# Kernel optimization log

Measured on AMD Instinct MI355X. Metric: run time of the kernel, lower is better.

The kernel has to match this reference:

```python
import jax, jax.numpy as jnp
import numpy as np

TOP_K = 4
N_GROUP = 4
TOPK_GROUP = 2
ROUTED_SCALING = 1.0


def setup_inputs() -> dict:
    key = jax.random.key(0)
    k1, k2, k3, k4, k5 = jax.random.split(key, 5)
    B, S, H, I, E = 1, 2048, 1024, 512, 16
    hidden_states = jax.random.normal(k1, (B, S, H), dtype=jnp.float32)
    # router weight (kaiming-uniform-like scale)
    gate_weight = jax.random.normal(k2, (E, H), dtype=jnp.float32) * (1.0 / np.sqrt(H))
    e_bias = jnp.zeros((E,), dtype=jnp.float32)  # e_score_correction_bias buffer
    gate_proj = jax.random.normal(k3, (E, I, H), dtype=jnp.float32) * 0.02
    up_proj = jax.random.normal(k4, (E, I, H), dtype=jnp.float32) * 0.02
    down_proj = jax.random.normal(k5, (E, H, I), dtype=jnp.float32) * 0.02
    return {
        "hidden_states": hidden_states,
        "gate_weight": gate_weight,
        "e_bias": e_bias,
        "gate_proj": gate_proj,
        "up_proj": up_proj,
        "down_proj": down_proj,
    }


def _route(x_flat, gate_weight, e_bias):
    # x_flat: [T, H]
    T = x_flat.shape[0]
    E = gate_weight.shape[0]
    logits = jnp.einsum("th,eh->te", x_flat, gate_weight)
    scores = jax.nn.sigmoid(logits)                      # [T, E]
    scores_for_choice = scores + e_bias[None, :]
    # group scores = sum of top-2 expert scores within each group
    grp = scores_for_choice.reshape(T, N_GROUP, E // N_GROUP)
    top2, _ = jax.lax.top_k(grp, 2)
    group_scores = top2.sum(axis=-1)                     # [T, G]
    _, group_idx = jax.lax.top_k(group_scores, TOPK_GROUP)
    group_mask = jax.nn.one_hot(group_idx, N_GROUP, dtype=scores.dtype).sum(axis=1)  # [T, G]
    score_mask = jnp.repeat(group_mask, E // N_GROUP, axis=1)                        # [T, E]
    tmp_scores = jnp.where(score_mask > 0, scores_for_choice, 0.0)
    _, topk_idx = jax.lax.top_k(tmp_scores, TOP_K)       # [T, K]
    topk_weight = jnp.take_along_axis(scores, topk_idx, axis=1)
    denom = topk_weight.sum(axis=-1, keepdims=True) + 1e-20
    topk_weight = topk_weight / denom * ROUTED_SCALING
    return topk_idx, topk_weight


def reference(hidden_states, gate_weight, e_bias, gate_proj, up_proj, down_proj):
    B, S, H = hidden_states.shape
    E = gate_proj.shape[0]
    x = hidden_states.reshape(-1, H).astype(jnp.float32)  # [T, H]
    topk_idx, topk_weight = _route(x, gate_weight, e_bias)
    # combine weights per (token, expert): sum over the k slots selecting e
    combine = (jax.nn.one_hot(topk_idx, E, dtype=x.dtype) * topk_weight[..., None]).sum(axis=1)  # [T, E]
    # dense expert MLP (mathematically equal to gather-compute-scatter since
    # non-selected experts receive zero combine weight)
    g = jnp.einsum("th,eih->tei", x, gate_proj)
    u = jnp.einsum("th,eih->tei", x, up_proj)
    act = jax.nn.silu(g) * u                              # [T, E, I]
    expert_out = jnp.einsum("tei,ehi->teh", act, down_proj)
    y = jnp.einsum("teh,te->th", expert_out, combine)
    return y.reshape(B, S, H)
```

## Files before the change

### kernel.cpp

```cpp
#include <hip/hip_runtime.h>
#include <hip/hip_bf16.h>

typedef __attribute__((ext_vector_type(8))) short bf16x8;
typedef __attribute__((ext_vector_type(4))) float f32x4;

#define T_TOK 2048
#define HD 1024
#define ID 512
#define NE 16
#define TOPK 4
#define BK 64
#define WELEM (HD*ID*NE)

__device__ __forceinline__ unsigned pk2(float a, float b) {
    return __builtin_amdgcn_perm(__float_as_uint(b), __float_as_uint(a),
                                 0x07060302u);
}
__device__ __forceinline__ bf16x8 cvt8(const float* __restrict__ p) {
    float4 a = *(const float4*)p;
    float4 b = *(const float4*)(p + 4);
    union { bf16x8 v; unsigned u[4]; } r;
    r.u[0] = pk2(a.x, a.y); r.u[1] = pk2(a.z, a.w);
    r.u[2] = pk2(b.x, b.y); r.u[3] = pk2(b.z, b.w);
    return r.v;
}
__device__ __forceinline__ short f2bf(float f) {
    unsigned u = __float_as_uint(f);
    return (short)((u + 0x7fffu + ((u >> 16) & 1u)) >> 16);
}

#define MFMA_BF16 __builtin_amdgcn_mfma_f32_16x16x32_bf16

__global__ __launch_bounds__(256) void conv_k(const float* __restrict__ src,
                                              short* __restrict__ dst) {
    size_t i = ((size_t)blockIdx.x * 256 + threadIdx.x) * 8;
    union { bf16x8 v; uint4 q; } r;
    r.v = cvt8(src + i);
    *(uint4*)(dst + i) = r.q;
}

__global__ __launch_bounds__(256) void router_k(
        const float* __restrict__ x, const float* __restrict__ gw,
        const float* __restrict__ eb,
        int* __restrict__ tk_idx, float* __restrict__ tk_w,
        short* __restrict__ xb) {
    int wid  = (blockIdx.x * 256 + threadIdx.x) >> 6;
    int lane = threadIdx.x & 63;

    const float* xr = x + (size_t)wid * HD + lane * 16;
    float xv[16];
#pragma unroll
    for (int c = 0; c < 4; c++) {
        float4 v = *(const float4*)(xr + c * 4);
        xv[4 * c] = v.x; xv[4 * c + 1] = v.y; xv[4 * c + 2] = v.z; xv[4 * c + 3] = v.w;
    }
    {
        union { uint4 q; unsigned u[4]; } w0, w1;
        w0.u[0] = pk2(xv[0], xv[1]);  w0.u[1] = pk2(xv[2], xv[3]);
        w0.u[2] = pk2(xv[4], xv[5]);  w0.u[3] = pk2(xv[6], xv[7]);
        w1.u[0] = pk2(xv[8], xv[9]);  w1.u[1] = pk2(xv[10], xv[11]);
        w1.u[2] = pk2(xv[12], xv[13]); w1.u[3] = pk2(xv[14], xv[15]);
        short* d = xb + ((size_t)wid << 10) + lane * 16;
        *(uint4*)d = w0.q;
        *(uint4*)(d + 8) = w1.q;
    }

    float logits[NE];
#pragma unroll
    for (int e = 0; e < NE; e++) {
        const float* gr = gw + e * HD + lane * 16;
        float p = 0.f;
#pragma unroll
        for (int c = 0; c < 4; c++) {
            float4 v = *(const float4*)(gr + c * 4);
            p += xv[4 * c] * v.x + xv[4 * c + 1] * v.y +
                 xv[4 * c + 2] * v.z + xv[4 * c + 3] * v.w;
        }
#pragma unroll
        for (int s = 32; s > 0; s >>= 1) p += __shfl_xor(p, s, 64);
        logits[e] = p;
    }

    float scores[NE], sc[NE];
#pragma unroll
    for (int e = 0; e < NE; e++) {
        scores[e] = 1.f / (1.f + __expf(-logits[e]));
        sc[e] = scores[e] + eb[e];
    }

    float gs[4];
#pragma unroll
    for (int g = 0; g < 4; g++) {
        float a = sc[4 * g], b = sc[4 * g + 1], c = sc[4 * g + 2], d = sc[4 * g + 3];
        float h1 = fmaxf(a, b), l1 = fminf(a, b);
        float h2 = fmaxf(c, d), l2 = fminf(c, d);
        gs[g] = fmaxf(h1, h2) + fmaxf(fminf(h1, h2), fmaxf(l1, l2));
    }
    int g0 = 0; float b0 = gs[0];
#pragma unroll
    for (int g = 1; g < 4; g++) if (gs[g] > b0) { b0 = gs[g]; g0 = g; }
    int g1 = -1; float b1 = -1e30f;
#pragma unroll
    for (int g = 0; g < 4; g++) if (g != g0 && gs[g] > b1) { b1 = gs[g]; g1 = g; }

    int taken = 0;
    int bid[TOPK]; float bsc[TOPK]; float wsum = 0.f;
#pragma unroll
    for (int k = 0; k < TOPK; k++) {
        float bv = -1e30f; int bi = 0; float bs = 0.f;
#pragma unroll
        for (int e = 0; e < NE; e++) {
            int grp = e >> 2;
            bool ok = ((grp == g0) || (grp == g1)) && !((taken >> e) & 1);
            if (ok && sc[e] > bv) { bv = sc[e]; bi = e; bs = scores[e]; }
        }
        taken |= (1 << bi);
        bid[k] = bi; bsc[k] = bs; wsum += bs;
    }
    if (lane == 0) {
        float inv = 1.0f / (wsum + 1e-20f);
#pragma unroll
        for (int k = 0; k < TOPK; k++) {
            tk_idx[wid * TOPK + k] = bid[k];
            tk_w[wid * TOPK + k]   = bsc[k] * inv;
        }
    }
}

__global__ __launch_bounds__(256) void assign_k(
        const int* __restrict__ tk_idx,
        int* __restrict__ counts, int* __restrict__ tok_list,
        int* __restrict__ pair_slot) {
    int p = blockIdx.x * 256 + threadIdx.x;
    int e = tk_idx[p];
    int slot = atomicAdd(&counts[e], 1);
    tok_list[e * T_TOK + slot] = p >> 2;
    pair_slot[p] = slot;
}

__global__ void offs_k(const int* __restrict__ counts, int* __restrict__ offs) {
    if (threadIdx.x == 0) {
        int a = 0;
#pragma unroll
        for (int e = 0; e < NE; e++) { offs[e] = a; a += counts[e]; }
    }
}

__global__ __launch_bounds__(256) void gemm1_k(
        const short* __restrict__ xb,
        const short* __restrict__ gpb,
        const short* __restrict__ upb,
        const int* __restrict__ counts,
        const int* __restrict__ offs,
        const int* __restrict__ tok_list,
        short* __restrict__ act) {
    __shared__ short xs[128 * BK];
    __shared__ short gs[64 * BK];
    __shared__ short us[64 * BK];
    __shared__ int   tok_s[128];

    int e = blockIdx.z;
    int cnt = counts[e];
    int base = blockIdx.y * 128;
    if (base >= cnt) return;
    int arow0 = offs[e] + base;

    int tid = threadIdx.x;
    if (tid < 128) {
        int s = base + tid;
        tok_s[tid] = (s < cnt) ? tok_list[e * T_TOK + s] : tok_list[e * T_TOK];
    }

    int wv = tid >> 6, lane = tid & 63;
    int qd = lane >> 4, l16 = lane & 15;
    int wm = (wv >> 1) * 64, wn = (wv & 1) * 32;
    int nb0 = blockIdx.x * 64;
    const short* gp = gpb + (size_t)e * ID * HD + (size_t)nb0 * HD;
    const short* up = upb + (size_t)e * ID * HD + (size_t)nb0 * HD;

    f32x4 accg[4][2] = {};
    f32x4 accu[4][2] = {};
    __syncthreads();

    for (int kp = 0; kp < HD; kp += BK) {
#pragma unroll
        for (int i = 0; i < 4; i++) {
            int idx = i * 256 + tid;
            int r = idx >> 3, c = idx & 7;
            *(uint4*)&xs[(r << 6) + (((c ^ r) & 7) << 3)] =
                *(const uint4*)(xb + ((size_t)tok_s[r] << 10) + kp + (c << 3));
        }
#pragma unroll
        for (int i = 0; i < 2; i++) {
            int idx = i * 256 + tid;
            int r = idx >> 3, c = idx & 7;
            size_t go = (size_t)r * HD + kp + (c << 3);
            int lo = (r << 6) + (((c ^ r) & 7) << 3);
            *(uint4*)&gs[lo] = *(const uint4*)(gp + go);
            *(uint4*)&us[lo] = *(const uint4*)(up + go);
        }
        __syncthreads();
#pragma unroll
        for (int ks = 0; ks < 2; ks++) {
            int cb = ks * 4 + qd;
            bf16x8 af[4], bg[2], bu[2];
#pragma unroll
            for (int i = 0; i < 4; i++) {
                int r = wm + i * 16 + l16;
                af[i] = *(const bf16x8*)&xs[(r << 6) + (((cb ^ r) & 7) << 3)];
            }
#pragma unroll
            for (int j = 0; j < 2; j++) {
                int r = wn + j * 16 + l16;
                int lo = (r << 6) + (((cb ^ r) & 7) << 3);
                bg[j] = *(const bf16x8*)&gs[lo];
                bu[j] = *(const bf16x8*)&us[lo];
            }
#pragma unroll
            for (int i = 0; i < 4; i++)
#pragma unroll
                for (int j = 0; j < 2; j++) {
                    accg[i][j] = MFMA_BF16(af[i], bg[j], accg[i][j], 0, 0, 0);
                    accu[i][j] = MFMA_BF16(af[i], bu[j], accu[i][j], 0, 0, 0);
                }
        }
        __syncthreads();
    }

#pragma unroll
    for (int i = 0; i < 4; i++)
#pragma unroll
        for (int j = 0; j < 2; j++)
#pragma unroll
            for (int r = 0; r < 4; r++) {
                int m = wm + i * 16 + qd * 4 + r;
                if (base + m < cnt) {
                    float g = accg[i][j][r], u = accu[i][j][r];
                    float a = g / (1.f + __expf(-g)) * u;
                    act[(size_t)(arow0 + m) * ID + nb0 + wn + j * 16 + l16] = f2bf(a);
                }
            }
}

__global__ __launch_bounds__(256) void gemm2_k(
        const short* __restrict__ act,
        const short* __restrict__ dpb,
        const int* __restrict__ counts,
        const int* __restrict__ offs,
        float* __restrict__ yexp) {
    __shared__ short as_[128 * BK];
    __shared__ short ds_[128 * BK];

    int e = blockIdx.z;
    int cnt = counts[e];
    int base = blockIdx.y * 128;
    if (base >= cnt) return;
    int arow0 = offs[e] + base;

    int tid = threadIdx.x;
    int wv = tid >> 6, lane = tid & 63;
    int qd = lane >> 4, l16 = lane & 15;
    int wm = (wv >> 1) * 64, wn = (wv & 1) * 64;
    int hb0 = blockIdx.x * 128;
    const short* dp = dpb + (size_t)e * HD * ID + (size_t)hb0 * ID;

    f32x4 acc[4][4] = {};
    __syncthreads();

    for (int kp = 0; kp < ID; kp += BK) {
#pragma unroll
        for (int i = 0; i < 4; i++) {
            int idx = i * 256 + tid;
            int r = idx >> 3, c = idx & 7;
            int lo = (r << 6) + (((c ^ r) & 7) << 3);
            *(uint4*)&as_[lo] =
                *(const uint4*)(act + (size_t)(arow0 + r) * ID + kp + (c << 3));
            *(uint4*)&ds_[lo] =
                *(const uint4*)(dp + (size_t)r * ID + kp + (c << 3));
        }
        __syncthreads();
#pragma unroll
        for (int ks = 0; ks < 2; ks++) {
            int cb = ks * 4 + qd;
            bf16x8 af[4], bd[4];
#pragma unroll
            for (int i = 0; i < 4; i++) {
                int r = wm + i * 16 + l16;
                af[i] = *(const bf16x8*)&as_[(r << 6) + (((cb ^ r) & 7) << 3)];
                int r2 = wn + i * 16 + l16;
                bd[i] = *(const bf16x8*)&ds_[(r2 << 6) + (((cb ^ r2) & 7) << 3)];
            }
#pragma unroll
            for (int i = 0; i < 4; i++)
#pragma unroll
                for (int j = 0; j < 4; j++)
                    acc[i][j] = MFMA_BF16(af[i], bd[j], acc[i][j], 0, 0, 0);
        }
        __syncthreads();
    }

#pragma unroll
    for (int i = 0; i < 4; i++)
#pragma unroll
        for (int j = 0; j < 4; j++)
#pragma unroll
            for (int r = 0; r < 4; r++) {
                int m = wm + i * 16 + qd * 4 + r;
                if (base + m < cnt)
                    yexp[(size_t)(arow0 + m) * HD + hb0 + wn + j * 16 + l16] =
                        acc[i][j][r];
            }
}

__global__ __launch_bounds__(256) void combine_k(
        const float* __restrict__ yexp,
        const int* __restrict__ offs,
        const int* __restrict__ tk_idx, const float* __restrict__ tk_w,
        const int* __restrict__ pair_slot,
        float* __restrict__ out) {
    int t = blockIdx.x, i = threadIdx.x;
    float4 acc = {0.f, 0.f, 0.f, 0.f};
#pragma unroll
    for (int k = 0; k < TOPK; k++) {
        int p = t * TOPK + k;
        int e = tk_idx[p];
        int row = offs[e] + pair_slot[p];
        float w = tk_w[p];
        float4 v = *(const float4*)(yexp + (size_t)row * HD + (i << 2));
        acc.x += w * v.x; acc.y += w * v.y;
        acc.z += w * v.z; acc.w += w * v.w;
    }
    *(float4*)(out + (size_t)t * HD + (i << 2)) = acc;
}

extern "C" void kernel_launch(void* const* d_in, const int* in_sizes, int n_in,
                              void* d_out, int out_size, void* d_ws, size_t ws_size,
                              hipStream_t stream) {
    const float* x  = (const float*)d_in[0];
    const float* gw = (const float*)d_in[1];
    const float* eb = (const float*)d_in[2];
    const float* gp = (const float*)d_in[3];
    const float* up = (const float*)d_in[4];
    const float* dp = (const float*)d_in[5];

    short* gpb = (short*)d_ws;
    short* upb = gpb + WELEM;
    short* dpb = upb + WELEM;
    short* xb  = dpb + WELEM;
    short* act = xb + (size_t)T_TOK * HD;
    int* counts    = (int*)(act + (size_t)(T_TOK * TOPK + 128) * ID);
    int* offs      = counts + NE;
    int* tok_list  = offs + NE;
    int* pair_slot = tok_list + NE * T_TOK;
    int* tk_idx    = pair_slot + T_TOK * TOPK;
    float* tk_w    = (float*)(tk_idx + T_TOK * TOPK);
    float* yexp = (float*)gpb;

    hipMemsetAsync(counts, 0, NE * sizeof(int), stream);
    hipMemsetAsync(d_out, 0, (size_t)out_size * sizeof(float), stream);

    conv_k<<<WELEM / 8 / 256, 256, 0, stream>>>(gp, gpb);
    conv_k<<<WELEM / 8 / 256, 256, 0, stream>>>(up, upb);
    conv_k<<<WELEM / 8 / 256, 256, 0, stream>>>(dp, dpb);
    router_k<<<T_TOK / 4, 256, 0, stream>>>(x, gw, eb, tk_idx, tk_w, xb);
    assign_k<<<T_TOK * TOPK / 256, 256, 0, stream>>>(tk_idx, counts,
                                                     tok_list, pair_slot);
    offs_k<<<1, 64, 0, stream>>>(counts, offs);
    gemm1_k<<<dim3(ID / 64, T_TOK / 128, NE), 256, 0, stream>>>(
        xb, gpb, upb, counts, offs, tok_list, act);
    gemm2_k<<<dim3(HD / 128, T_TOK / 128, NE), 256, 0, stream>>>(
        act, dpb, counts, offs, yexp);
    combine_k<<<T_TOK, 256, 0, stream>>>(yexp, offs, tk_idx, tk_w,
                                         pair_slot, (float*)d_out);
}
```

Baseline: 255.2 us.

## Use direct global-to-LDS loads, merge weight conversions, store expert outputs as bf16

The GEMM tile loads now use global_load_lds, which writes straight into shared memory without passing through registers. The swizzle moves to the global address side, and the load addresses are precomputed once outside the K loop. The three weight-conversion launches become one 2D-grid launch, and the redundant output memset is removed. Expert outputs are stored as bf16 instead of fp32, which halves yexp traffic; the combine kernel reads them as bf16, handles two tokens per block, and does wider loads. Keeping intermediates in bf16 costs some precision.

```diff
diff --git a/kernel.cpp b/kernel.cpp
--- a/kernel.cpp
+++ b/kernel.cpp
@@ -28,11 +28,23 @@
     unsigned u = __float_as_uint(f);
     return (short)((u + 0x7fffu + ((u >> 16) & 1u)) >> 16);
 }
+__device__ __forceinline__ float bf2f(short s) {
+    return __uint_as_float(((unsigned)(unsigned short)s) << 16);
+}
+__device__ __forceinline__ void load_lds16(const short* g, short* l) {
+    __builtin_amdgcn_global_load_lds(
+        (const __attribute__((address_space(1))) unsigned*)g,
+        (__attribute__((address_space(3))) unsigned*)l, 16, 0, 0);
+}
 
 #define MFMA_BF16 __builtin_amdgcn_mfma_f32_16x16x32_bf16
 
-__global__ __launch_bounds__(256) void conv_k(const float* __restrict__ src,
-                                              short* __restrict__ dst) {
+__global__ __launch_bounds__(256) void conv_k(
+        const float* __restrict__ s0, short* __restrict__ d0,
+        const float* __restrict__ s1, short* __restrict__ d1,
+        const float* __restrict__ s2, short* __restrict__ d2) {
+    const float* src = (blockIdx.y == 0) ? s0 : (blockIdx.y == 1) ? s1 : s2;
+    short* dst       = (blockIdx.y == 0) ? d0 : (blockIdx.y == 1) ? d1 : d2;
     size_t i = ((size_t)blockIdx.x * 256 + threadIdx.x) * 8;
     union { bf16x8 v; uint4 q; } r;
     r.v = cvt8(src + i);
@@ -170,6 +182,7 @@
         int s = base + tid;
         tok_s[tid] = (s < cnt) ? tok_list[e * T_TOK + s] : tok_list[e * T_TOK];
     }
+    __syncthreads();
 
     int wv = tid >> 6, lane = tid & 63;
     int qd = lane >> 4, l16 = lane & 15;
@@ -178,26 +191,34 @@
     const short* gp = gpb + (size_t)e * ID * HD + (size_t)nb0 * HD;
     const short* up = upb + (size_t)e * ID * HD + (size_t)nb0 * HD;
 
+    const short* xsg[4]; short* xld[4];
+#pragma unroll
+    for (int i = 0; i < 4; i++) {
+        int idx = i * 256 + tid, r = idx >> 3, c = idx & 7;
+        xsg[i] = xb + ((size_t)tok_s[r] << 10) + (((c ^ r) & 7) << 3);
+        xld[i] = &xs[(i * 256 + wv * 64) * 8];
+    }
+    const short* gsg[2]; const short* usg[2]; short* gld[2]; short* uld[2];
+#pragma unroll
+    for (int i = 0; i < 2; i++) {
+        int idx = i * 256 + tid, r = idx >> 3, c = idx & 7;
+        size_t so = (size_t)r * HD + (((c ^ r) & 7) << 3);
+        gsg[i] = gp + so;
+        usg[i] = up + so;
+        gld[i] = &gs[(i * 256 + wv * 64) * 8];
+        uld[i] = &us[(i * 256 + wv * 64) * 8];
+    }
+
     f32x4 accg[4][2] = {};
     f32x4 accu[4][2] = {};
-    __syncthreads();
 
     for (int kp = 0; kp < HD; kp += BK) {
 #pragma unroll
-        for (int i = 0; i < 4; i++) {
-            int idx = i * 256 + tid;
-            int r = idx >> 3, c = idx & 7;
-            *(uint4*)&xs[(r << 6) + (((c ^ r) & 7) << 3)] =
-                *(const uint4*)(xb + ((size_t)tok_s[r] << 10) + kp + (c << 3));
-        }
+        for (int i = 0; i < 4; i++) load_lds16(xsg[i] + kp, xld[i]);
 #pragma unroll
         for (int i = 0; i < 2; i++) {
-            int idx = i * 256 + tid;
-            int r = idx >> 3, c = idx & 7;
-            size_t go = (size_t)r * HD + kp + (c << 3);
-            int lo = (r << 6) + (((c ^ r) & 7) << 3);
-            *(uint4*)&gs[lo] = *(const uint4*)(gp + go);
-            *(uint4*)&us[lo] = *(const uint4*)(up + go);
+            load_lds16(gsg[i] + kp, gld[i]);
+            load_lds16(usg[i] + kp, uld[i]);
         }
         __syncthreads();
 #pragma unroll
@@ -247,7 +268,7 @@
         const short* __restrict__ dpb,
         const int* __restrict__ counts,
         const int* __restrict__ offs,
-        float* __restrict__ yexp) {
+        short* __restrict__ yexp) {
     __shared__ short as_[128 * BK];
     __shared__ short ds_[128 * BK];
 
@@ -264,19 +285,24 @@
     int hb0 = blockIdx.x * 128;
     const short* dp = dpb + (size_t)e * HD * ID + (size_t)hb0 * ID;
 
+    const short* asg[4]; const short* dsg[4]; short* ald[4]; short* dld[4];
+#pragma unroll
+    for (int i = 0; i < 4; i++) {
+        int idx = i * 256 + tid, r = idx >> 3, c = idx & 7;
+        int sw = ((c ^ r) & 7) << 3;
+        asg[i] = act + (size_t)(arow0 + r) * ID + sw;
+        dsg[i] = dp + (size_t)r * ID + sw;
+        ald[i] = &as_[(i * 256 + wv * 64) * 8];
+        dld[i] = &ds_[(i * 256 + wv * 64) * 8];
+    }
+
     f32x4 acc[4][4] = {};
-    __syncthreads();
 
     for (int kp = 0; kp < ID; kp += BK) {
 #pragma unroll
         for (int i = 0; i < 4; i++) {
-            int idx = i * 256 + tid;
-            int r = idx >> 3, c = idx & 7;
-            int lo = (r << 6) + (((c ^ r) & 7) << 3);
-            *(uint4*)&as_[lo] =
-                *(const uint4*)(act + (size_t)(arow0 + r) * ID + kp + (c << 3));
-            *(uint4*)&ds_[lo] =
-                *(const uint4*)(dp + (size_t)r * ID + kp + (c << 3));
+            load_lds16(asg[i] + kp, ald[i]);
+            load_lds16(dsg[i] + kp, dld[i]);
         }
         __syncthreads();
 #pragma unroll
@@ -308,29 +334,34 @@
                 int m = wm + i * 16 + qd * 4 + r;
                 if (base + m < cnt)
                     yexp[(size_t)(arow0 + m) * HD + hb0 + wn + j * 16 + l16] =
-                        acc[i][j][r];
+                        f2bf(acc[i][j][r]);
             }
 }
 
 __global__ __launch_bounds__(256) void combine_k(
-        const float* __restrict__ yexp,
+        const short* __restrict__ yexp,
         const int* __restrict__ offs,
         const int* __restrict__ tk_idx, const float* __restrict__ tk_w,
         const int* __restrict__ pair_slot,
         float* __restrict__ out) {
-    int t = blockIdx.x, i = threadIdx.x;
-    float4 acc = {0.f, 0.f, 0.f, 0.f};
+    int t = blockIdx.x * 2 + (threadIdx.x >> 7);
+    int i = threadIdx.x & 127;
+    float acc[8] = {};
 #pragma unroll
     for (int k = 0; k < TOPK; k++) {
         int p = t * TOPK + k;
         int e = tk_idx[p];
         int row = offs[e] + pair_slot[p];
         float w = tk_w[p];
-        float4 v = *(const float4*)(yexp + (size_t)row * HD + (i << 2));
-        acc.x += w * v.x; acc.y += w * v.y;
-        acc.z += w * v.z; acc.w += w * v.w;
-    }
-    *(float4*)(out + (size_t)t * HD + (i << 2)) = acc;
+        bf16x8 v = *(const bf16x8*)(yexp + (size_t)row * HD + i * 8);
+#pragma unroll
+        for (int j = 0; j < 8; j++) acc[j] += w * bf2f(v[j]);
+    }
+    float4 o0 = {acc[0], acc[1], acc[2], acc[3]};
+    float4 o1 = {acc[4], acc[5], acc[6], acc[7]};
+    float* d = out + (size_t)t * HD + i * 8;
+    *(float4*)d = o0;
+    *(float4*)(d + 4) = o1;
 }
 
 extern "C" void kernel_launch(void* const* d_in, const int* in_sizes, int n_in,
@@ -354,14 +385,12 @@
     int* pair_slot = tok_list + NE * T_TOK;
     int* tk_idx    = pair_slot + T_TOK * TOPK;
     float* tk_w    = (float*)(tk_idx + T_TOK * TOPK);
-    float* yexp = (float*)gpb;
+    short* yexp = gpb;
 
     hipMemsetAsync(counts, 0, NE * sizeof(int), stream);
-    hipMemsetAsync(d_out, 0, (size_t)out_size * sizeof(float), stream);
-
-    conv_k<<<WELEM / 8 / 256, 256, 0, stream>>>(gp, gpb);
-    conv_k<<<WELEM / 8 / 256, 256, 0, stream>>>(up, upb);
-    conv_k<<<WELEM / 8 / 256, 256, 0, stream>>>(dp, dpb);
+
+    conv_k<<<dim3(WELEM / 8 / 256, 3), 256, 0, stream>>>(gp, gpb, up, upb,
+                                                         dp, dpb);
     router_k<<<T_TOK / 4, 256, 0, stream>>>(x, gw, eb, tk_idx, tk_w, xb);
     assign_k<<<T_TOK * TOPK / 256, 256, 0, stream>>>(tk_idx, counts,
                                                      tok_list, pair_slot);
@@ -370,6 +399,6 @@
         xb, gpb, upb, counts, offs, tok_list, act);
     gemm2_k<<<dim3(HD / 128, T_TOK / 128, NE), 256, 0, stream>>>(
         act, dpb, counts, offs, yexp);
-    combine_k<<<T_TOK, 256, 0, stream>>>(yexp, offs, tk_idx, tk_w,
-                                         pair_slot, (float*)d_out);
-}
+    combine_k<<<T_TOK / 2, 256, 0, stream>>>(yexp, offs, tk_idx, tk_w,
+                                             pair_slot, (float*)d_out);
+}
```

Result: faster. 245.0 us (-4.0%).
